# Kernel optimization log

Measured on AMD Instinct MI355X. Metric: run time of the kernel, lower is better.

Reference implementation:

```python
import jax, jax.numpy as jnp
import numpy as np

N_NODES = 50000
N_EDGES = 1000000
F = 64


def setup_inputs() -> dict:
    key = jax.random.key(0)
    k1, k2, k3, k4, k5 = jax.random.split(key, 5)
    nodes = jax.random.normal(k1, (N_NODES, F), dtype=jnp.float32)
    edges = jax.random.normal(k2, (N_EDGES, F), dtype=jnp.float32)
    edge_index = jax.random.randint(k3, (2, N_EDGES), 0, N_NODES, dtype=jnp.int64)
    edge_pairs = jax.random.randint(k4, (1, N_EDGES), 0, N_EDGES, dtype=jnp.int64)
    return {"nodes": nodes, "edges": edges, "edge_index": edge_index, "edge_pairs": edge_pairs}


def reference(nodes, edges, edge_index, edge_pairs):
    # AggregateLocalEdges(scatter_sum): sum edge messages into receiving node (edge_index[0])
    pooled = jax.ops.segment_sum(edges, edge_index[0], num_segments=nodes.shape[0])  # [N, F]
    # GatherNodesOutgoing: gather pooled node features back onto edges at edge_index[1]
    ed_new = pooled[edge_index[1]]  # [M, F]
    # GatherEdgesPairs: gather reverse-edge message
    ed_not = edges[edge_pairs[0]]  # [M, F]
    # Subtract
    return ed_new - ed_not
```

## Files before the change

### kernel.cpp

```cpp
#include <hip/hip_runtime.h>

#define FDIM 64

__global__ void dmpnn_scatter_add(const float* __restrict__ edges,
                                  const int* __restrict__ recv,
                                  float* __restrict__ pooled,
                                  long long total ) {
    long long tid = (long long)blockIdx.x * blockDim.x + threadIdx.x;
    if (tid >= total) return;
    int e = (int)(tid >> 6);
    int f = (int)(tid & 63);
    float v = edges[tid];
    int node = recv[e];
    atomicAdd(&pooled[(long long)node * FDIM + f], v);
}

__global__ void dmpnn_gather_sub(const float* __restrict__ pooled,
                                 const float* __restrict__ edges,
                                 const int* __restrict__ send,
                                 const int* __restrict__ pair,
                                 float* __restrict__ out,
                                 long long total ) {
    long long tid = (long long)blockIdx.x * blockDim.x + threadIdx.x;
    if (tid >= total) return;
    int e = (int)(tid >> 4);
    int q = (int)(tid & 15);
    int sn = send[e];
    int pe = pair[e];
    float4 a = *reinterpret_cast<const float4*>(&pooled[(long long)sn * FDIM + q * 4]);
    float4 b = *reinterpret_cast<const float4*>(&edges[(long long)pe * FDIM + q * 4]);
    float4 r;
    r.x = a.x - b.x;
    r.y = a.y - b.y;
    r.z = a.z - b.z;
    r.w = a.w - b.w;
    *reinterpret_cast<float4*>(&out[tid * 4]) = r;
}

extern "C" void kernel_launch(void* const* d_in, const int* in_sizes, int n_in,
                              void* d_out, int out_size, void* d_ws, size_t ws_size,
                              hipStream_t stream) {
    const float* edges      = (const float*)d_in[1];
    const int*   edge_index = (const int*)d_in[2];
    const int*   edge_pairs = (const int*)d_in[3];

    const int N = in_sizes[0] / FDIM;
    const int M = in_sizes[1] / FDIM;

    float* pooled = (float*)d_ws;

    hipMemsetAsync(pooled, 0, (size_t)N * FDIM * sizeof(float), stream);

    {
        long long total = (long long)M * FDIM;
        int blk = 256;
        long long grid = (total + blk - 1) / blk;
        dmpnn_scatter_add<<<dim3((unsigned)grid), dim3(blk), 0, stream>>>(
            edges, edge_index, pooled, total);
    }

    {
        long long total = (long long)M * (FDIM / 4);
        int blk = 256;
        long long grid = (total + blk - 1) / blk;
        dmpnn_gather_sub<<<dim3((unsigned)grid), dim3(blk), 0, stream>>>(
            pooled, edges, edge_index + M, edge_pairs, (float*)d_out, total);
    }
}
```

Measured before the change: 326.4 us.

## Replace atomic scatter-add with CSR-sorted segmented aggregation

Builds a CSR index from the receiver array with a histogram, a single-block scan and an atomic fill pass. The per-node sum is then computed with one wave per node reading its incoming edges, with no atomics. This removes 64M float atomics on pooled and adds four extra kernels, including a serial single-block scan over 50k nodes and 1M int atomics. The old path stays as a fallback when the workspace is too small.

```diff
diff --git a/kernel.cpp b/kernel.cpp
--- a/kernel.cpp
+++ b/kernel.cpp
@@ -5,7 +5,7 @@
 __global__ void dmpnn_scatter_add(const float* __restrict__ edges,
                                   const int* __restrict__ recv,
                                   float* __restrict__ pooled,
-                                  long long total ) {
+                                  long long total) {
     long long tid = (long long)blockIdx.x * blockDim.x + threadIdx.x;
     if (tid >= total) return;
     int e = (int)(tid >> 6);
@@ -15,12 +15,71 @@
     atomicAdd(&pooled[(long long)node * FDIM + f], v);
 }
 
+__global__ void dmpnn_hist(const int* __restrict__ recv, int* __restrict__ counts, int M) {
+    int e = blockIdx.x * blockDim.x + threadIdx.x;
+    if (e >= M) return;
+    atomicAdd(&counts[recv[e]], 1);
+}
+
+__global__ void dmpnn_scan(const int* __restrict__ counts,
+                           int* __restrict__ offsets,
+                           int* __restrict__ cursor, int N) {
+    __shared__ int part[1024];
+    int t = threadIdx.x;
+    int chunk = (N + 1023) >> 10;
+    int lo = t * chunk;
+    int hi = lo + chunk; if (hi > N) hi = N; if (lo > N) lo = N;
+    int s = 0;
+    for (int i = lo; i < hi; ++i) s += counts[i];
+    part[t] = s;
+    __syncthreads();
+    for (int d = 1; d < 1024; d <<= 1) {
+        int v = (t >= d) ? part[t - d] : 0;
+        __syncthreads();
+        part[t] += v;
+        __syncthreads();
+    }
+    int base = (t == 0) ? 0 : part[t - 1];
+    for (int i = lo; i < hi; ++i) {
+        offsets[i] = base;
+        cursor[i]  = base;
+        base += counts[i];
+    }
+    if (t == 1023) offsets[N] = part[1023];
+}
+
+__global__ void dmpnn_fill(const int* __restrict__ recv,
+                           int* __restrict__ cursor,
+                           int* __restrict__ perm, int M) {
+    int e = blockIdx.x * blockDim.x + threadIdx.x;
+    if (e >= M) return;
+    int pos = atomicAdd(&cursor[recv[e]], 1);
+    perm[pos] = e;
+}
+
+__global__ void dmpnn_aggregate(const float* __restrict__ edges,
+                                const int* __restrict__ perm,
+                                const int* __restrict__ offsets,
+                                float* __restrict__ pooled, int N) {
+    int wave = (int)(((long long)blockIdx.x * blockDim.x + threadIdx.x) >> 6);
+    int lane = threadIdx.x & 63;
+    if (wave >= N) return;
+    int lo = offsets[wave];
+    int hi = offsets[wave + 1];
+    float acc = 0.0f;
+    for (int j = lo; j < hi; ++j) {
+        int e = perm[j];
+        acc += edges[(long long)e * FDIM + lane];
+    }
+    pooled[(long long)wave * FDIM + lane] = acc;
+}
+
 __global__ void dmpnn_gather_sub(const float* __restrict__ pooled,
                                  const float* __restrict__ edges,
                                  const int* __restrict__ send,
                                  const int* __restrict__ pair,
                                  float* __restrict__ out,
-                                 long long total ) {
+                                 long long total) {
     long long tid = (long long)blockIdx.x * blockDim.x + threadIdx.x;
     if (tid >= total) return;
     int e = (int)(tid >> 4);
@@ -47,23 +106,42 @@
     const int N = in_sizes[0] / FDIM;
     const int M = in_sizes[1] / FDIM;
 
-    float* pooled = (float*)d_ws;
+    size_t need = ((size_t)(3 * N + 1) + (size_t)M) * sizeof(int)
+                + (size_t)N * FDIM * sizeof(float);
 
-    hipMemsetAsync(pooled, 0, (size_t)N * FDIM * sizeof(float), stream);
+    const int* recv = edge_index;
+    const int* send = edge_index + M;
 
-    {
-        long long total = (long long)M * FDIM;
-        int blk = 256;
-        long long grid = (total + blk - 1) / blk;
-        dmpnn_scatter_add<<<dim3((unsigned)grid), dim3(blk), 0, stream>>>(
-            edges, edge_index, pooled, total);
-    }
+    if (ws_size >= need) {
+        int*   counts  = (int*)d_ws;
+        int*   offsets = counts + N;
+        int*   cursor  = offsets + (N + 1);
+        int*   perm    = cursor + N;
+        float* pooled  = (float*)(perm + M);
 
-    {
+        hipMemsetAsync(counts, 0, (size_t)N * sizeof(int), stream);
+
+        dmpnn_hist<<<dim3((M + 255) / 256), dim3(256), 0, stream>>>(recv, counts, M);
+        dmpnn_scan<<<dim3(1), dim3(1024), 0, stream>>>(counts, offsets, cursor, N);
+        dmpnn_fill<<<dim3((M + 255) / 256), dim3(256), 0, stream>>>(recv, cursor, perm, M);
+
+        {
+            int wavesPerBlock = 4;
+            int grid = (N + wavesPerBlock - 1) / wavesPerBlock;
+            dmpnn_aggregate<<<dim3(grid), dim3(256), 0, stream>>>(edges, perm, offsets, pooled, N);
+        }
+
         long long total = (long long)M * (FDIM / 4);
-        int blk = 256;
-        long long grid = (total + blk - 1) / blk;
-        dmpnn_gather_sub<<<dim3((unsigned)grid), dim3(blk), 0, stream>>>(
-            pooled, edges, edge_index + M, edge_pairs, (float*)d_out, total);
+        dmpnn_gather_sub<<<dim3((unsigned)((total + 255) / 256)), dim3(256), 0, stream>>>(
+            pooled, edges, send, edge_pairs, (float*)d_out, total);
+    } else {
+        float* pooled = (float*)d_ws;
+        hipMemsetAsync(pooled, 0, (size_t)N * FDIM * sizeof(float), stream);
+        long long totalS = (long long)M * FDIM;
+        dmpnn_scatter_add<<<dim3((unsigned)((totalS + 255) / 256)), dim3(256), 0, stream>>>(
+            edges, recv, pooled, totalS);
+        long long total = (long long)M * (FDIM / 4);
+        dmpnn_gather_sub<<<dim3((unsigned)((total + 255) / 256)), dim3(256), 0, stream>>>(
+            pooled, edges, send, edge_pairs, (float*)d_out, total);
     }
 }
```

Measured after the change: 494.5 us. +51.5%, slower.

## Sort edges by receiver and pre-reduce runs before atomic scatter

Applied to the files above, without the earlier changes.

Replaces the per-element atomic scatter-add with a counting sort of edges by receiving node (histogram, block scan with global atomic allocation, fill), then an aggregate kernel that sums runs of same-node edges in registers before issuing atomics. The aim is fewer float atomics. It also adds nontemporal loads and stores. The cost is three extra passes over the index arrays plus more workspace. With about 20 edges per node, each 16-edge group mostly holds one or two nodes. The old path is kept as a fallback when the workspace is too small.

```diff
diff --git a/kernel.cpp b/kernel.cpp
--- a/kernel.cpp
+++ b/kernel.cpp
@@ -1,11 +1,15 @@
 #include <hip/hip_runtime.h>
 
 #define FDIM 64
+#define BLK 256
+
+typedef float f32x4 __attribute__((ext_vector_type(4)));
+typedef int   i32x4 __attribute__((ext_vector_type(4)));
 
 __global__ void dmpnn_scatter_add(const float* __restrict__ edges,
                                   const int* __restrict__ recv,
                                   float* __restrict__ pooled,
-                                  long long total ) {
+                                  long long total) {
     long long tid = (long long)blockIdx.x * blockDim.x + threadIdx.x;
     if (tid >= total) return;
     int e = (int)(tid >> 6);
@@ -15,26 +19,117 @@
     atomicAdd(&pooled[(long long)node * FDIM + f], v);
 }
 
-__global__ void dmpnn_gather_sub(const float* __restrict__ pooled,
-                                 const float* __restrict__ edges,
+__global__ void dmpnn_hist(const int* __restrict__ recv, int* __restrict__ counts, int M) {
+    int e = blockIdx.x * blockDim.x + threadIdx.x;
+    if (e >= M) return;
+    atomicAdd(&counts[recv[e]], 1);
+}
+
+__global__ void dmpnn_alloc(const int* __restrict__ counts,
+                            int* __restrict__ cursor,
+                            int* __restrict__ gcounter, int N) {
+    __shared__ int s[BLK];
+    __shared__ int sbase;
+    int t = blockIdx.x * BLK + threadIdx.x;
+    int c = (t < N) ? counts[t] : 0;
+    s[threadIdx.x] = c;
+    __syncthreads();
+    for (int d = 1; d < BLK; d <<= 1) {
+        int v = (threadIdx.x >= (unsigned)d) ? s[threadIdx.x - d] : 0;
+        __syncthreads();
+        s[threadIdx.x] += v;
+        __syncthreads();
+    }
+    if (threadIdx.x == BLK - 1) sbase = atomicAdd(gcounter, s[BLK - 1]);
+    __syncthreads();
+    if (t < N) cursor[t] = sbase + s[threadIdx.x] - c;
+}
+
+__global__ void dmpnn_fill(const int* __restrict__ recv,
+                           int* __restrict__ cursor,
+                           int* __restrict__ perm,
+                           int* __restrict__ nodeOf, int M) {
+    int e = blockIdx.x * blockDim.x + threadIdx.x;
+    if (e >= M) return;
+    int n = recv[e];
+    int pos = atomicAdd(&cursor[n], 1);
+    perm[pos] = e;
+    nodeOf[pos] = n;
+}
+
+__global__ void dmpnn_aggregate(const float* __restrict__ edges,
+                                const int* __restrict__ perm,
+                                const int* __restrict__ nodeOf,
+                                float* __restrict__ pooled, int M) {
+    const f32x4* edges4 = (const f32x4*)edges;
+    long long tid = (long long)blockIdx.x * blockDim.x + threadIdx.x;
+    int grp = (int)(tid >> 4);
+    int q   = (int)(tid & 15);
+    int g0  = grp << 4;
+    if (g0 >= M) return;
+    int cnt = M - g0; if (cnt > 16) cnt = 16;
+
+    const i32x4* p4 = (const i32x4*)(perm + g0);
+    const i32x4* n4 = (const i32x4*)(nodeOf + g0);
+    i32x4 pa = p4[0], pb = p4[1], pc = p4[2], pd = p4[3];
+    i32x4 na = n4[0], nb = n4[1], nc = n4[2], nd = n4[3];
+    int ee[16] = {pa.x, pa.y, pa.z, pa.w, pb.x, pb.y, pb.z, pb.w,
+                  pc.x, pc.y, pc.z, pc.w, pd.x, pd.y, pd.z, pd.w};
+    int nn[16] = {na.x, na.y, na.z, na.w, nb.x, nb.y, nb.z, nb.w,
+                  nc.x, nc.y, nc.z, nc.w, nd.x, nd.y, nd.z, nd.w};
+
+    f32x4 v[16];
+    #pragma unroll
+    for (int k = 0; k < 16; ++k) {
+        int e = (k < cnt) ? ee[k] : ee[0];
+        v[k] = __builtin_nontemporal_load(&edges4[(long long)e * 16 + q]);
+    }
+
+    f32x4 acc = v[0];
+    int curn = nn[0];
+    #pragma unroll
+    for (int k = 1; k < 16; ++k) {
+        if (k < cnt) {
+            if (nn[k] == curn) {
+                acc += v[k];
+            } else {
+                float* dst = &pooled[(long long)curn * FDIM + (q << 2)];
+                atomicAdd(dst + 0, acc.x);
+                atomicAdd(dst + 1, acc.y);
+                atomicAdd(dst + 2, acc.z);
+                atomicAdd(dst + 3, acc.w);
+                acc = v[k];
+                curn = nn[k];
+            }
+        }
+    }
+    float* dst = &pooled[(long long)curn * FDIM + (q << 2)];
+    atomicAdd(dst + 0, acc.x);
+    atomicAdd(dst + 1, acc.y);
+    atomicAdd(dst + 2, acc.z);
+    atomicAdd(dst + 3, acc.w);
+}
+
+__global__ void dmpnn_gather_sub(const float4* __restrict__ pooled4,
+                                 const float4* __restrict__ edges4,
                                  const int* __restrict__ send,
                                  const int* __restrict__ pair,
-                                 float* __restrict__ out,
-                                 long long total ) {
+                                 float4* __restrict__ out4,
+                                 long long total) {
     long long tid = (long long)blockIdx.x * blockDim.x + threadIdx.x;
     if (tid >= total) return;
     int e = (int)(tid >> 4);
     int q = (int)(tid & 15);
     int sn = send[e];
     int pe = pair[e];
-    float4 a = *reinterpret_cast<const float4*>(&pooled[(long long)sn * FDIM + q * 4]);
-    float4 b = *reinterpret_cast<const float4*>(&edges[(long long)pe * FDIM + q * 4]);
-    float4 r;
+    float4 a = pooled4[(long long)sn * 16 + q];
+    float4 b = edges4[(long long)pe * 16 + q];
+    f32x4 r;
     r.x = a.x - b.x;
     r.y = a.y - b.y;
     r.z = a.z - b.z;
     r.w = a.w - b.w;
-    *reinterpret_cast<float4*>(&out[tid * 4]) = r;
+    __builtin_nontemporal_store(r, (f32x4*)&out4[tid]);
 }
 
 extern "C" void kernel_launch(void* const* d_in, const int* in_sizes, int n_in,
@@ -47,23 +142,49 @@
     const int N = in_sizes[0] / FDIM;
     const int M = in_sizes[1] / FDIM;
 
-    float* pooled = (float*)d_ws;
+    const int* recv = edge_index;
+    const int* send = edge_index + M;
 
-    hipMemsetAsync(pooled, 0, (size_t)N * FDIM * sizeof(float), stream);
+    const size_t Np = (size_t)((N + 3) & ~3);
+    const size_t Mp = (size_t)((M + 3) & ~3);
 
-    {
-        long long total = (long long)M * FDIM;
-        int blk = 256;
-        long long grid = (total + blk - 1) / blk;
-        dmpnn_scatter_add<<<dim3((unsigned)grid), dim3(blk), 0, stream>>>(
-            edges, edge_index, pooled, total);
-    }
+    size_t need = (2 * Np + 4 + 2 * Mp) * sizeof(int)
+                + (size_t)N * FDIM * sizeof(float);
 
-    {
+    if (ws_size >= need) {
+        int*   counts   = (int*)d_ws;
+        int*   gcounter = counts + Np;
+        int*   cursor   = gcounter + 4;
+        int*   perm     = cursor + Np;
+        int*   nodeOf   = perm + Mp;
+        float* pooled   = (float*)(nodeOf + Mp);
+
+        (void)hipMemsetAsync(counts, 0, (Np + 4) * sizeof(int), stream);
+        (void)hipMemsetAsync(pooled, 0, (size_t)N * FDIM * sizeof(float), stream);
+
+        dmpnn_hist<<<dim3((M + BLK - 1) / BLK), dim3(BLK), 0, stream>>>(recv, counts, M);
+        dmpnn_alloc<<<dim3((N + BLK - 1) / BLK), dim3(BLK), 0, stream>>>(counts, cursor, gcounter, N);
+        dmpnn_fill<<<dim3((M + BLK - 1) / BLK), dim3(BLK), 0, stream>>>(recv, cursor, perm, nodeOf, M);
+
+        {
+            long long threads = ((long long)(M + 15) / 16) * 16;
+            dmpnn_aggregate<<<dim3((unsigned)((threads + BLK - 1) / BLK)), dim3(BLK), 0, stream>>>(
+                edges, perm, nodeOf, pooled, M);
+        }
+
         long long total = (long long)M * (FDIM / 4);
-        int blk = 256;
-        long long grid = (total + blk - 1) / blk;
-        dmpnn_gather_sub<<<dim3((unsigned)grid), dim3(blk), 0, stream>>>(
-            pooled, edges, edge_index + M, edge_pairs, (float*)d_out, total);
+        dmpnn_gather_sub<<<dim3((unsigned)((total + BLK - 1) / BLK)), dim3(BLK), 0, stream>>>(
+            (const float4*)pooled, (const float4*)edges, send, edge_pairs,
+            (float4*)d_out, total);
+    } else {
+        float* pooled = (float*)d_ws;
+        (void)hipMemsetAsync(pooled, 0, (size_t)N * FDIM * sizeof(float), stream);
+        long long totalS = (long long)M * FDIM;
+        dmpnn_scatter_add<<<dim3((unsigned)((totalS + BLK - 1) / BLK)), dim3(BLK), 0, stream>>>(
+            edges, recv, pooled, totalS);
+        long long total = (long long)M * (FDIM / 4);
+        dmpnn_gather_sub<<<dim3((unsigned)((total + BLK - 1) / BLK)), dim3(BLK), 0, stream>>>(
+            (const float4*)pooled, (const float4*)edges, send, edge_pairs,
+            (float4*)d_out, total);
     }
 }
```

Measured after the change: 386.4 us. +18.4%, slower.
